# Kernel tuning notes

Measured on AMD Instinct MI355X. Metric: run time of the kernel, lower is better.

The kernel has to match this reference:

```python
import jax, jax.numpy as jnp
import numpy as np

OOV_INDEX = 1  # stand-in for params.OOV_INDEX
H = 1024
VOCAB = 50000
L = 2048


def setup_inputs() -> dict:
    key = jax.random.key(0)
    ks = jax.random.split(key, 10)
    s = 0.05
    inp = {
        "input_ids": jax.random.randint(ks[0], (L,), 0, VOCAB),
        "embedding": jax.random.normal(ks[1], (VOCAB, H), jnp.float32) * s,
        "fwd_W_ih": jax.random.normal(ks[2], (3 * H, H), jnp.float32) * s,
        "fwd_W_hh": jax.random.normal(ks[3], (3 * H, H), jnp.float32) * s,
        "fwd_b_ih": jax.random.normal(ks[4], (3 * H,), jnp.float32) * s,
        "fwd_b_hh": jax.random.normal(ks[5], (3 * H,), jnp.float32) * s,
        "rev_W_ih": jax.random.normal(ks[6], (3 * H, H), jnp.float32) * s,
        "rev_W_hh": jax.random.normal(ks[7], (3 * H, H), jnp.float32) * s,
        "rev_b_ih": jax.random.normal(ks[8], (3 * H,), jnp.float32) * s,
        "rev_b_hh": jax.random.normal(ks[9], (3 * H,), jnp.float32) * s,
    }
    return inp


def _gru_scan(x_seq, W_ih, W_hh, b_ih, b_hh):
    # x_seq: [L, H]. PyTorch GRU gate order: r, z, n.
    gx = x_seq @ W_ih.T + b_ih  # [L, 3H], input projections precomputed

    def step(h, gx_t):
        gh = h @ W_hh.T + b_hh
        gx_r, gx_z, gx_n = jnp.split(gx_t, 3)
        gh_r, gh_z, gh_n = jnp.split(gh, 3)
        r = jax.nn.sigmoid(gx_r + gh_r)
        z = jax.nn.sigmoid(gx_z + gh_z)
        n = jnp.tanh(gx_n + r * gh_n)
        h_new = (1.0 - z) * n + z * h
        return h_new, h_new

    h0 = jnp.zeros((x_seq.shape[1],), x_seq.dtype)
    h_last, outs = jax.lax.scan(step, h0, gx)
    return outs, h_last  # [L, H], [H]


def reference(input_ids, embedding, fwd_W_ih, fwd_W_hh, fwd_b_ih, fwd_b_hh,
              rev_W_ih, rev_W_hh, rev_b_ih, rev_b_hh):
    # Embedding lookup; OOV index -> zero vector (empty_vector in original)
    embeds = embedding[input_ids]  # [L, H]
    embeds = jnp.where((input_ids == OOV_INDEX)[:, None], 0.0, embeds)

    fwd_outputs, fwd_h = _gru_scan(embeds, fwd_W_ih, fwd_W_hh, fwd_b_ih, fwd_b_hh)
    rev_outs_rev, rev_h = _gru_scan(embeds[::-1], rev_W_ih, rev_W_hh, rev_b_ih, rev_b_hh)
    rev_outputs = rev_outs_rev[::-1]  # place back at original positions

    outputs = jnp.concatenate([fwd_outputs, rev_outputs], axis=1)  # [L, 2H]
    hidden = jnp.concatenate([fwd_h, rev_h])[None, None, :]        # [1, 1, 2H]
    projected_output = hidden
    return outputs, hidden, projected_output
```

## Files before the change

kernel.cpp:

```cpp
#include <hip/hip_runtime.h>
#include <math.h>

#define SEQL 2048
#define H 1024
#define G3 3072
#define SENT 1.0e30f

__device__ __forceinline__ float sigmoidf_(float x){ return 1.0f/(1.0f+expf(-x)); }

__device__ __forceinline__ float4 ld_cohere4(const float* p){
  float4 r;
  asm volatile("global_load_dwordx4 %0, %1, off sc0 sc1\n\t"
               "s_waitcnt vmcnt(0)"
               : "=&v"(r) : "v"(p) : "memory");
  return r;
}
__device__ __forceinline__ void st_cohere1(float* p, float v){
  asm volatile("global_store_dword %0, %1, off sc0 sc1"
               :: "v"(p), "v"(v) : "memory");
}

__global__ __launch_bounds__(256) void init_sent(float* p, int n4){
  int i = blockIdx.x*256 + threadIdx.x;
  if (i < n4) ((float4*)p)[i] = make_float4(SENT,SENT,SENT,SENT);
}

__global__ __launch_bounds__(256) void embed_kernel(const int* __restrict__ ids,
                                                    const float* __restrict__ emb,
                                                    float* __restrict__ out){
  int t = blockIdx.x;
  int id = ids[t];
  const float4* src = (const float4*)(emb + (size_t)id*H);
  float4* dst = (float4*)(out + (size_t)t*H);
  float4 v = (id == 1) ? make_float4(0.f,0.f,0.f,0.f) : src[threadIdx.x];
  dst[threadIdx.x] = v;
}

__global__ __launch_bounds__(256) void gemm_kernel(const float* __restrict__ A,
  const float* __restrict__ WF, const float* __restrict__ WR,
  const float* __restrict__ bF, const float* __restrict__ bR,
  float* __restrict__ gxF, float* __restrict__ gxR)
{
  __shared__ float As[16][68];
  __shared__ float Bs[16][68];
  const int tid = threadIdx.x;
  const int n0 = blockIdx.x * 64;
  const int m0 = blockIdx.y * 64;
  const int dir = (n0 >= G3);
  const float* B    = dir ? WR : WF;
  const float* bias = dir ? bR : bF;
  float* C          = dir ? gxR : gxF;
  const int j0 = dir ? (n0 - G3) : n0;

  const int lr = tid >> 2;
  const int lc = (tid & 3) * 4;
  const int tx = tid & 15;
  const int ty = tid >> 4;

  float acc[4][4] = {};

  for (int k0 = 0; k0 < H; k0 += 16){
    float4 av = *(const float4*)(A + (size_t)(m0+lr)*H + k0 + lc);
    float4 bv = *(const float4*)(B + (size_t)(j0+lr)*H + k0 + lc);
    As[lc+0][lr]=av.x; As[lc+1][lr]=av.y; As[lc+2][lr]=av.z; As[lc+3][lr]=av.w;
    Bs[lc+0][lr]=bv.x; Bs[lc+1][lr]=bv.y; Bs[lc+2][lr]=bv.z; Bs[lc+3][lr]=bv.w;
    __syncthreads();
    #pragma unroll
    for (int kk=0; kk<16; ++kk){
      float a0=As[kk][ty*4+0], a1=As[kk][ty*4+1], a2=As[kk][ty*4+2], a3=As[kk][ty*4+3];
      float b0=Bs[kk][tx*4+0], b1=Bs[kk][tx*4+1], b2=Bs[kk][tx*4+2], b3=Bs[kk][tx*4+3];
      acc[0][0]=fmaf(a0,b0,acc[0][0]); acc[0][1]=fmaf(a0,b1,acc[0][1]);
      acc[0][2]=fmaf(a0,b2,acc[0][2]); acc[0][3]=fmaf(a0,b3,acc[0][3]);
      acc[1][0]=fmaf(a1,b0,acc[1][0]); acc[1][1]=fmaf(a1,b1,acc[1][1]);
      acc[1][2]=fmaf(a1,b2,acc[1][2]); acc[1][3]=fmaf(a1,b3,acc[1][3]);
      acc[2][0]=fmaf(a2,b0,acc[2][0]); acc[2][1]=fmaf(a2,b1,acc[2][1]);
      acc[2][2]=fmaf(a2,b2,acc[2][2]); acc[2][3]=fmaf(a2,b3,acc[2][3]);
      acc[3][0]=fmaf(a3,b0,acc[3][0]); acc[3][1]=fmaf(a3,b1,acc[3][1]);
      acc[3][2]=fmaf(a3,b2,acc[3][2]); acc[3][3]=fmaf(a3,b3,acc[3][3]);
    }
    __syncthreads();
  }

  #pragma unroll
  for (int u=0; u<4; ++u){
    float4 o;
    o.x = acc[u][0] + bias[j0+tx*4+0];
    o.y = acc[u][1] + bias[j0+tx*4+1];
    o.z = acc[u][2] + bias[j0+tx*4+2];
    o.w = acc[u][3] + bias[j0+tx*4+3];
    *(float4*)(C + (size_t)(m0+ty*4+u)*G3 + j0 + tx*4) = o;
  }
}

__global__ __launch_bounds__(512, 1) void scan_kernel(
  const float* __restrict__ gxF, const float* __restrict__ gxR,
  const float* __restrict__ WhF, const float* __restrict__ WhR,
  const float* __restrict__ bhF, const float* __restrict__ bhR,
  float* hFbuf, float* hRbuf, float* __restrict__ out)
{
  const int wgid = blockIdx.x;
  const int dir  = wgid >> 7;
  const int d    = wgid & 127;
  const int i0   = d * 8;
  const int tid  = threadIdx.x;
  const int lane = tid & 63;
  const int wv   = tid >> 6;

  const float* gx  = dir ? gxR : gxF;
  const float* Whh = dir ? WhR : WhF;
  const float* bhh = dir ? bhR : bhF;
  float* hbuf      = dir ? hRbuf : hFbuf;

  const int ia = i0 + wv;
  const int rows[3] = { ia, H+ia, 2*H+ia };

  float wa[48];
  float bias[3];
  #pragma unroll
  for (int rr=0; rr<3; ++rr){
    bias[rr] = bhh[rows[rr]];
    const float* wp = Whh + (size_t)rows[rr]*H;
    #pragma unroll
    for (int q=0; q<4; ++q){
      float4 w4 = *(const float4*)(wp + q*256 + lane*4);
      asm volatile("v_accvgpr_write_b32 %0, %1" : "=a"(wa[rr*16+q*4+0]) : "v"(w4.x));
      asm volatile("v_accvgpr_write_b32 %0, %1" : "=a"(wa[rr*16+q*4+1]) : "v"(w4.y));
      asm volatile("v_accvgpr_write_b32 %0, %1" : "=a"(wa[rr*16+q*4+2]) : "v"(w4.z));
      asm volatile("v_accvgpr_write_b32 %0, %1" : "=a"(wa[rr*16+q*4+3]) : "v"(w4.w));
    }
  }

  __shared__ float hs[2][H];

  for (int s=0; s<SEQL; ++s){
    const int b = s & 1;
    const int t = dir ? (SEQL-1-s) : s;
    const float* gxt = gx + (size_t)t*G3;
    float g0 = gxt[ia], g1 = gxt[H+ia], g2 = gxt[2*H+ia];
    float wr[48];
    #pragma unroll
    for (int i=0; i<48; ++i)
      asm volatile("v_accvgpr_read_b32 %0, %1" : "=v"(wr[i]) : "a"(wa[i]));

    if (tid < 256){
      float4* dst = (float4*)&hs[b][tid*4];
      if (s == 0){
        *dst = make_float4(0.f,0.f,0.f,0.f);
      } else {
        const float* src = hbuf + (size_t)(s-1)*H + tid*4;
        float4 v;
        do { v = ld_cohere4(src); }
        while (v.x==SENT || v.y==SENT || v.z==SENT || v.w==SENT);
        *dst = v;
      }
    }
    __syncthreads();

    float hv[16];
    #pragma unroll
    for (int q=0; q<4; ++q){
      float4 hq = *(const float4*)&hs[b][q*256 + lane*4];
      hv[q*4+0]=hq.x; hv[q*4+1]=hq.y; hv[q*4+2]=hq.z; hv[q*4+3]=hq.w;
    }

    float dots[3];
    #pragma unroll
    for (int rr=0; rr<3; ++rr){
      float acc = 0.f;
      #pragma unroll
      for (int m=0; m<16; ++m) acc = fmaf(wr[rr*16+m], hv[m], acc);
      #pragma unroll
      for (int off=32; off>0; off>>=1) acc += __shfl_xor(acc, off);
      dots[rr] = acc + bias[rr];
    }

    const float hp = hs[b][ia];
    float r = sigmoidf_(g0 + dots[0]);
    float z = sigmoidf_(g1 + dots[1]);
    float n = tanhf    (g2 + r*dots[2]);
    float hn = (1.f - z)*n + z*hp;

    if (lane == 0){
      st_cohere1(hbuf + (size_t)s*H + ia, hn);
      out[(size_t)t*2048 + dir*H + ia] = hn;
      if (s == SEQL-1){
        const size_t base = (size_t)SEQL*2048;
        out[base + dir*H + ia]        = hn;
        out[base + 2048 + dir*H + ia] = hn;
      }
    }
  }
}

extern "C" void kernel_launch(void* const* d_in, const int* in_sizes, int n_in,
                              void* d_out, int out_size, void* d_ws, size_t ws_size,
                              hipStream_t stream)
{
  const int*   ids  = (const int*)  d_in[0];
  const float* emb  = (const float*)d_in[1];
  const float* WihF = (const float*)d_in[2];
  const float* WhhF = (const float*)d_in[3];
  const float* bihF = (const float*)d_in[4];
  const float* bhhF = (const float*)d_in[5];
  const float* WihR = (const float*)d_in[6];
  const float* WhhR = (const float*)d_in[7];
  const float* bihR = (const float*)d_in[8];
  const float* bhhR = (const float*)d_in[9];
  float* out = (float*)d_out;
  float* ws  = (float*)d_ws;

  float* embeds = ws;
  float* gxF    = embeds + (size_t)SEQL*H;
  float* gxR    = gxF + (size_t)SEQL*G3;
  float* hF     = gxR + (size_t)SEQL*G3;
  float* hR     = hF + (size_t)SEQL*H;

  init_sent<<<4096, 256, 0, stream>>>(hF, 1048576);
  embed_kernel<<<SEQL, 256, 0, stream>>>(ids, emb, embeds);
  dim3 gg(96, 32);
  gemm_kernel<<<gg, 256, 0, stream>>>(embeds, WihF, WihR, bihF, bihR, gxF, gxR);
  scan_kernel<<<256, 512, 0, stream>>>(gxF, gxR, WhhF, WhhR, bhhF, bhhR, hF, hR, out);
}
```

Baseline: 7.014 ms.

## Replace sentinel polling with per-step atomic counters for cross-block hidden-state sync

Instead of each block spinning on the 1024-float hidden vector until no sentinel value remains, each block now stages its 8 outputs in shared memory, writes them with one thread, and then increments one of 8 padded per-step atomic counters. Consumers poll only those 8 counters until each reaches 16, then load the hidden vector once. This aims to cut polling traffic and removes the sentinel initialization of the whole hidden buffer. The cost is an extra __syncthreads per step and a serialized store-then-atomic by a single thread.

Result: faster. 6.409 ms (-8.6%).

```diff
diff --git a/kernel.cpp b/kernel.cpp
--- a/kernel.cpp
+++ b/kernel.cpp
@@ -4,7 +4,6 @@
 #define SEQL 2048
 #define H 1024
 #define G3 3072
-#define SENT 1.0e30f
 
 __device__ __forceinline__ float sigmoidf_(float x){ return 1.0f/(1.0f+expf(-x)); }
 
@@ -15,14 +14,21 @@
                : "=&v"(r) : "v"(p) : "memory");
   return r;
 }
-__device__ __forceinline__ void st_cohere1(float* p, float v){
-  asm volatile("global_store_dword %0, %1, off sc0 sc1"
+__device__ __forceinline__ int ld_ctr(const int* p){
+  int r;
+  asm volatile("global_load_dword %0, %1, off sc0 sc1\n\t"
+               "s_waitcnt vmcnt(0)"
+               : "=&v"(r) : "v"(p) : "memory");
+  return r;
+}
+__device__ __forceinline__ void st_cohere2(float* p, float2 v){
+  asm volatile("global_store_dwordx2 %0, %1, off sc0 sc1"
                :: "v"(p), "v"(v) : "memory");
 }
 
-__global__ __launch_bounds__(256) void init_sent(float* p, int n4){
+__global__ __launch_bounds__(256) void init_zero(int* p, int n4){
   int i = blockIdx.x*256 + threadIdx.x;
-  if (i < n4) ((float4*)p)[i] = make_float4(SENT,SENT,SENT,SENT);
+  if (i < n4) ((int4*)p)[i] = make_int4(0,0,0,0);
 }
 
 __global__ __launch_bounds__(256) void embed_kernel(const int* __restrict__ ids,
@@ -96,7 +102,8 @@
   const float* __restrict__ gxF, const float* __restrict__ gxR,
   const float* __restrict__ WhF, const float* __restrict__ WhR,
   const float* __restrict__ bhF, const float* __restrict__ bhR,
-  float* hFbuf, float* hRbuf, float* __restrict__ out)
+  float* hFbuf, float* hRbuf, int* ctrF, int* ctrR,
+  float* __restrict__ out)
 {
   const int wgid = blockIdx.x;
   const int dir  = wgid >> 7;
@@ -110,6 +117,7 @@
   const float* Whh = dir ? WhR : WhF;
   const float* bhh = dir ? bhR : bhF;
   float* hbuf      = dir ? hRbuf : hFbuf;
+  int*   ctr       = dir ? ctrR : ctrF;
 
   const int ia = i0 + wv;
   const int rows[3] = { ia, H+ia, 2*H+ia };
@@ -131,6 +139,7 @@
   }
 
   __shared__ float hs[2][H];
+  __shared__ float hstage[2][8];
 
   for (int s=0; s<SEQL; ++s){
     const int b = s & 1;
@@ -142,17 +151,16 @@
     for (int i=0; i<48; ++i)
       asm volatile("v_accvgpr_read_b32 %0, %1" : "=v"(wr[i]) : "a"(wa[i]));
 
+    if (s > 0 && wv == 0 && lane < 8){
+      const int* cp = ctr + ((size_t)(s-1)*8 + lane)*16;
+      while (ld_ctr(cp) < 16) { }
+    }
+    __syncthreads();
+
     if (tid < 256){
-      float4* dst = (float4*)&hs[b][tid*4];
-      if (s == 0){
-        *dst = make_float4(0.f,0.f,0.f,0.f);
-      } else {
-        const float* src = hbuf + (size_t)(s-1)*H + tid*4;
-        float4 v;
-        do { v = ld_cohere4(src); }
-        while (v.x==SENT || v.y==SENT || v.z==SENT || v.w==SENT);
-        *dst = v;
-      }
+      float4 v = (s == 0) ? make_float4(0.f,0.f,0.f,0.f)
+                          : ld_cohere4(hbuf + (size_t)(s-1)*H + tid*4);
+      *(float4*)&hs[b][tid*4] = v;
     }
     __syncthreads();
 
@@ -162,7 +170,6 @@
       float4 hq = *(const float4*)&hs[b][q*256 + lane*4];
       hv[q*4+0]=hq.x; hv[q*4+1]=hq.y; hv[q*4+2]=hq.z; hv[q*4+3]=hq.w;
     }
-
     float dots[3];
     #pragma unroll
     for (int rr=0; rr<3; ++rr){
@@ -181,13 +188,25 @@
     float hn = (1.f - z)*n + z*hp;
 
     if (lane == 0){
-      st_cohere1(hbuf + (size_t)s*H + ia, hn);
+      hstage[b][wv] = hn;
       out[(size_t)t*2048 + dir*H + ia] = hn;
       if (s == SEQL-1){
         const size_t base = (size_t)SEQL*2048;
         out[base + dir*H + ia]        = hn;
         out[base + 2048 + dir*H + ia] = hn;
       }
+    }
+    __syncthreads();
+
+    if (tid == 0){
+      float* dst = hbuf + (size_t)s*H + i0;
+      st_cohere2(dst + 0, *(float2*)&hstage[b][0]);
+      st_cohere2(dst + 2, *(float2*)&hstage[b][2]);
+      st_cohere2(dst + 4, *(float2*)&hstage[b][4]);
+      st_cohere2(dst + 6, *(float2*)&hstage[b][6]);
+      asm volatile("s_waitcnt vmcnt(0)" ::: "memory");
+      __hip_atomic_fetch_add(ctr + ((size_t)s*8 + (d & 7))*16, 1,
+                             __ATOMIC_RELAXED, __HIP_MEMORY_SCOPE_AGENT);
     }
   }
 }
@@ -214,10 +233,13 @@
   float* gxR    = gxF + (size_t)SEQL*G3;
   float* hF     = gxR + (size_t)SEQL*G3;
   float* hR     = hF + (size_t)SEQL*H;
-
-  init_sent<<<4096, 256, 0, stream>>>(hF, 1048576);
+  int*   ctrF   = (int*)(hR + (size_t)SEQL*H);
+  int*   ctrR   = ctrF + (size_t)SEQL*8*16;
+
+  init_zero<<<512, 256, 0, stream>>>(ctrF, 131072);
   embed_kernel<<<SEQL, 256, 0, stream>>>(ids, emb, embeds);
   dim3 gg(96, 32);
   gemm_kernel<<<gg, 256, 0, stream>>>(embeds, WihF, WihR, bihF, bihR, gxF, gxR);
-  scan_kernel<<<256, 512, 0, stream>>>(gxF, gxR, WhhF, WhhR, bhhF, bhhR, hF, hR, out);
-}
+  scan_kernel<<<256, 512, 0, stream>>>(gxF, gxR, WhhF, WhhR, bhhF, bhhR,
+                                       hF, hR, ctrF, ctrR, out);
+}
```

## Reload recurrent weights per step and batch hidden-state publishing per workgroup

Applied to the files above, without the earlier changes.

The scan kernel stops holding W_hh rows in AGPRs and instead reloads them from global memory (expected to hit cache) every step. It raises the occupancy hint to two workgroups per CU. Each step now stages the eight new hidden values in shared memory and publishes them with one thread's four uncached 8-byte stores instead of eight separate lane stores. The workgroup reads its own previous values from shared memory rather than polling global memory. The trade is an extra barrier and per-step weight loads of about 12 KB per workgroup, in exchange for fewer coherent stores and less register pressure.

After: 8.285 ms. 18.1% more time.

```diff
diff --git a/kernel.cpp b/kernel.cpp
--- a/kernel.cpp
+++ b/kernel.cpp
@@ -8,15 +8,18 @@
 
 __device__ __forceinline__ float sigmoidf_(float x){ return 1.0f/(1.0f+expf(-x)); }
 
-__device__ __forceinline__ float4 ld_cohere4(const float* p){
+__device__ __forceinline__ float4 ld_uc(const float* p){
   float4 r;
   asm volatile("global_load_dwordx4 %0, %1, off sc0 sc1\n\t"
                "s_waitcnt vmcnt(0)"
                : "=&v"(r) : "v"(p) : "memory");
   return r;
 }
-__device__ __forceinline__ void st_cohere1(float* p, float v){
-  asm volatile("global_store_dword %0, %1, off sc0 sc1"
+__device__ __forceinline__ int ok4(float4 v){
+  return !(v.x==SENT || v.y==SENT || v.z==SENT || v.w==SENT);
+}
+__device__ __forceinline__ void st_uc_2(float* p, float2 v){
+  asm volatile("global_store_dwordx2 %0, %1, off sc0 sc1"
                :: "v"(p), "v"(v) : "memory");
 }
 
@@ -92,7 +95,7 @@
   }
 }
 
-__global__ __launch_bounds__(512, 1) void scan_kernel(
+__global__ __launch_bounds__(512, 2) void scan_kernel(
   const float* __restrict__ gxF, const float* __restrict__ gxR,
   const float* __restrict__ WhF, const float* __restrict__ WhR,
   const float* __restrict__ bhF, const float* __restrict__ bhR,
@@ -112,82 +115,90 @@
   float* hbuf      = dir ? hRbuf : hFbuf;
 
   const int ia = i0 + wv;
-  const int rows[3] = { ia, H+ia, 2*H+ia };
-
-  float wa[48];
-  float bias[3];
-  #pragma unroll
-  for (int rr=0; rr<3; ++rr){
-    bias[rr] = bhh[rows[rr]];
-    const float* wp = Whh + (size_t)rows[rr]*H;
-    #pragma unroll
-    for (int q=0; q<4; ++q){
-      float4 w4 = *(const float4*)(wp + q*256 + lane*4);
-      asm volatile("v_accvgpr_write_b32 %0, %1" : "=a"(wa[rr*16+q*4+0]) : "v"(w4.x));
-      asm volatile("v_accvgpr_write_b32 %0, %1" : "=a"(wa[rr*16+q*4+1]) : "v"(w4.y));
-      asm volatile("v_accvgpr_write_b32 %0, %1" : "=a"(wa[rr*16+q*4+2]) : "v"(w4.z));
-      asm volatile("v_accvgpr_write_b32 %0, %1" : "=a"(wa[rr*16+q*4+3]) : "v"(w4.w));
-    }
-  }
-
-  __shared__ float hs[2][H];
+  const float* wp0 = Whh + (size_t)(ia)*H;
+  const float* wp1 = Whh + (size_t)(H+ia)*H;
+  const float* wp2 = Whh + (size_t)(2*H+ia)*H;
+  const float b0v = bhh[ia], b1v = bhh[H+ia], b2v = bhh[2*H+ia];
+
+  __shared__ float hs[H];
+  __shared__ float hstage[2][8];
 
   for (int s=0; s<SEQL; ++s){
-    const int b = s & 1;
     const int t = dir ? (SEQL-1-s) : s;
     const float* gxt = gx + (size_t)t*G3;
     float g0 = gxt[ia], g1 = gxt[H+ia], g2 = gxt[2*H+ia];
-    float wr[48];
-    #pragma unroll
-    for (int i=0; i<48; ++i)
-      asm volatile("v_accvgpr_read_b32 %0, %1" : "=v"(wr[i]) : "a"(wa[i]));
+    float4 w0[4], w1[4], w2[4];
+    #pragma unroll
+    for (int q=0; q<4; ++q){
+      w0[q] = *(const float4*)(wp0 + q*256 + lane*4);
+      w1[q] = *(const float4*)(wp1 + q*256 + lane*4);
+      w2[q] = *(const float4*)(wp2 + q*256 + lane*4);
+    }
 
     if (tid < 256){
-      float4* dst = (float4*)&hs[b][tid*4];
-      if (s == 0){
-        *dst = make_float4(0.f,0.f,0.f,0.f);
-      } else {
+      float4 v;
+      if (s == 0)               v = make_float4(0.f,0.f,0.f,0.f);
+      else if ((tid >> 1) == d) v = *(const float4*)&hstage[(s-1)&1][(tid&1)*4];
+      else {
         const float* src = hbuf + (size_t)(s-1)*H + tid*4;
-        float4 v;
-        do { v = ld_cohere4(src); }
-        while (v.x==SENT || v.y==SENT || v.z==SENT || v.w==SENT);
-        *dst = v;
+        do { v = ld_uc(src); } while (!ok4(v));
       }
+      *(float4*)&hs[tid*4] = v;
     }
     __syncthreads();
 
     float hv[16];
     #pragma unroll
     for (int q=0; q<4; ++q){
-      float4 hq = *(const float4*)&hs[b][q*256 + lane*4];
+      float4 hq = *(const float4*)&hs[q*256 + lane*4];
       hv[q*4+0]=hq.x; hv[q*4+1]=hq.y; hv[q*4+2]=hq.z; hv[q*4+3]=hq.w;
     }
 
-    float dots[3];
-    #pragma unroll
-    for (int rr=0; rr<3; ++rr){
-      float acc = 0.f;
+    float d0=0.f, d1=0.f, d2=0.f;
+    #pragma unroll
+    for (int q=0; q<4; ++q){
+      const float* a0=(const float*)&w0[q];
+      const float* a1=(const float*)&w1[q];
+      const float* a2=(const float*)&w2[q];
       #pragma unroll
-      for (int m=0; m<16; ++m) acc = fmaf(wr[rr*16+m], hv[m], acc);
-      #pragma unroll
-      for (int off=32; off>0; off>>=1) acc += __shfl_xor(acc, off);
-      dots[rr] = acc + bias[rr];
-    }
-
-    const float hp = hs[b][ia];
-    float r = sigmoidf_(g0 + dots[0]);
-    float z = sigmoidf_(g1 + dots[1]);
-    float n = tanhf    (g2 + r*dots[2]);
+      for (int j=0; j<4; ++j){
+        float hj = hv[q*4+j];
+        d0 = fmaf(a0[j], hj, d0);
+        d1 = fmaf(a1[j], hj, d1);
+        d2 = fmaf(a2[j], hj, d2);
+      }
+    }
+    #pragma unroll
+    for (int off=32; off>0; off>>=1){
+      d0 += __shfl_xor(d0, off);
+      d1 += __shfl_xor(d1, off);
+      d2 += __shfl_xor(d2, off);
+    }
+
+    const float hp = hs[ia];
+    float r  = sigmoidf_(g0 + d0 + b0v);
+    float z  = sigmoidf_(g1 + d1 + b1v);
+    float n  = tanhf    (g2 + r*(d2 + b2v));
     float hn = (1.f - z)*n + z*hp;
 
     if (lane == 0){
-      st_cohere1(hbuf + (size_t)s*H + ia, hn);
+      hstage[s&1][wv] = hn;
       out[(size_t)t*2048 + dir*H + ia] = hn;
       if (s == SEQL-1){
         const size_t base = (size_t)SEQL*2048;
         out[base + dir*H + ia]        = hn;
         out[base + 2048 + dir*H + ia] = hn;
       }
+    }
+    __syncthreads();
+
+    if (tid == 0){
+      float* dst = hbuf + (size_t)s*H + i0;
+      const float* hv8 = &hstage[s&1][0];
+      st_uc_2(dst+0, make_float2(hv8[0], hv8[1]));
+      st_uc_2(dst+2, make_float2(hv8[2], hv8[3]));
+      st_uc_2(dst+4, make_float2(hv8[4], hv8[5]));
+      st_uc_2(dst+6, make_float2(hv8[6], hv8[7]));
     }
   }
 }
```
